# Kernel tuning notes

Hardware: AMD Instinct MI355X
Metric: run time of the kernel (lower is better)

Reference implementation:

```python
import jax, jax.numpy as jnp
import numpy as np

B, K, H, W = 8, 4, 256, 256
HID = 16
DT, STEPS, JITERS, OMEGA = 0.1, 12, 8, 0.9
D_MAX, CHI_MAX, K_MAX = 2.0, 2.0, 1.0


def _conv2d(x, w, b):
    y = jax.lax.conv_general_dilated(x, w, (1, 1), 'SAME',
                                     dimension_numbers=('NCHW', 'OIHW', 'NCHW'))
    return y + b[None, :, None, None]


def _pad(x):  # replicate pad by 1 on H, W
    return jnp.pad(x, ((0, 0), (0, 0), (1, 1), (1, 1)), mode='edge')


def laplacian(x):
    xp = _pad(x)
    return (xp[:, :, :-2, 1:-1] + xp[:, :, 2:, 1:-1]
            + xp[:, :, 1:-1, :-2] + xp[:, :, 1:-1, 2:] - 4.0 * x)


def gradient(x):
    xp = _pad(x)
    gx = xp[:, :, 1:-1, 2:] - x   # forward diff along W
    gy = xp[:, :, 2:, 1:-1] - x   # forward diff along H
    return gx, gy


def divergence(vx, vy):
    xp = _pad(vx)
    yp = _pad(vy)
    dvx = vx - xp[:, :, 1:-1, 2:]
    dvy = vy - yp[:, :, 2:, 1:-1]
    return dvx + dvy


def project_simplex(p, eps=1e-8):
    # p: [..., K]; faithful port incl. the rho-1 indexing of the torch code
    Kc = p.shape[-1]
    x = jnp.nan_to_num(p)
    u = jnp.flip(jnp.sort(x, axis=-1), axis=-1)            # descending
    cssv = jnp.cumsum(u, axis=-1) - 1.0
    ind = jnp.arange(1, Kc + 1, dtype=x.dtype)
    cond = (u - cssv / ind) > 0
    rho = jnp.argmax(cond.astype(jnp.int32) * jnp.arange(1, Kc + 1), axis=-1)
    rho_idx = jnp.maximum(rho - 1, 0)[..., None]
    tau = jnp.take_along_axis(cssv, rho_idx, axis=-1) / jnp.maximum(rho_idx + 1, 1)
    tau = jnp.nan_to_num(tau)
    w = jnp.maximum(x - tau, 0.0)
    return w / (w.sum(-1, keepdims=True) + eps)


def setup_inputs() -> dict:
    key = jax.random.key(0)
    ks = jax.random.split(key, 8)
    p0 = jax.random.uniform(ks[0], (B, K, H, W), dtype=jnp.float32)
    p0 = p0 / p0.sum(1, keepdims=True)
    w1 = jax.random.normal(ks[1], (HID, K, 3, 3), jnp.float32) * np.sqrt(2.0 / (K * 9))
    w2 = jax.random.normal(ks[2], (HID, HID, 3, 3), jnp.float32) * np.sqrt(2.0 / (HID * 9))
    w3 = jax.random.normal(ks[3], (1, HID, 1, 1), jnp.float32) * np.sqrt(1.0 / HID)
    return {
        'p0': p0,
        'D_raw': jnp.full((K,), 0.5, jnp.float32),
        'chi_raw': jnp.float32(0.5),
        'k_tumor_raw': jnp.float32(0.3),
        'cap_tumor_logit': jnp.float32(np.log(0.7) - np.log(0.3)),
        'w1': w1, 'b1': jnp.zeros((HID,), jnp.float32),
        'w2': w2, 'b2': jnp.zeros((HID,), jnp.float32),
        'w3': w3, 'b3': jnp.zeros((1,), jnp.float32),
        'tumor_idx': 0,
    }


def _forward(p0, D_raw, chi_raw, k_tumor_raw, cap_tumor_logit,
             w1, b1, w2, b2, w3, b3, tumor_idx):
    ti = int(tumor_idx)
    sp = jax.nn.softplus
    D_all = jnp.minimum(sp(D_raw) + 1e-8, D_MAX)                 # [K]
    chi = jnp.minimum(sp(chi_raw) + 1e-8, CHI_MAX)
    k_t = jnp.minimum(sp(k_tumor_raw) + 1e-8, K_MAX)             # unused in tumor_map mode
    cap_t = jnp.clip(jax.nn.sigmoid(cap_tumor_logit), 0.001, 0.95)

    # GrowthCNN (k_mode='tumor_map')
    h = jax.nn.relu(_conv2d(p0, w1, b1))
    h = jax.nn.relu(_conv2d(h, w2, b2))
    k_map = jnp.maximum(jax.nn.sigmoid(_conv2d(h, w3, b3)) * K_MAX, 1e-6)  # [B,1,H,W]

    D4 = D_all[None, :, None, None]
    diag = 1.0 + DT * D4 * 4.0

    p = jnp.maximum(jnp.nan_to_num(p0), 0.0)
    for _ in range(STEPS):
        gx, gy = gradient(p)
        gx = jnp.nan_to_num(gx)
        gy = jnp.nan_to_num(gy)
        sum_gx = gx.sum(1, keepdims=True)
        sum_gy = gy.sum(1, keepdims=True)
        fx = jnp.nan_to_num(-chi * p * (sum_gx - gx))
        fy = jnp.nan_to_num(-chi * p * (sum_gy - gy))
        cross = jnp.nan_to_num(divergence(fx, fy))

        pt = jnp.clip(p[:, ti:ti + 1], 0.0, 1.0)
        rt = jnp.nan_to_num(k_map * pt * (1.0 - pt / cap_t))
        react = jnp.zeros_like(p).at[:, ti:ti + 1].set(rt)

        rhs = jnp.nan_to_num(p + DT * (cross + react))

        # damped Jacobi for implicit diffusion, vectorized over channels
        xk = p
        for _it in range(JITERS):
            Lx = laplacian(xk)
            r = rhs - (xk - DT * D4 * Lx)
            xk = jnp.nan_to_num(xk + (OMEGA / diag) * r)

        p = project_simplex(jnp.moveaxis(xk, 1, -1))
        p = jnp.maximum(jnp.nan_to_num(jnp.moveaxis(p, -1, 1)), 0.0)
    return p


def reference(p0, D_raw, chi_raw, k_tumor_raw, cap_tumor_logit,
              w1, b1, w2, b2, w3, b3, tumor_idx):
    return _forward(p0, D_raw, chi_raw, k_tumor_raw, cap_tumor_logit,
                    w1, b1, w2, b2, w3, b3, tumor_idx)


if __name__ == '__main__':
    out = reference(**setup_inputs())
    print(out.shape, out.dtype)
```

## Files before the change

### kernel.cpp

```cpp
#include <hip/hip_runtime.h>
#include <math.h>

#define B_ 8
#define K4 4
#define H_ 256
#define W_ 256
#define HID_ 16
#define DT_ 0.1f
#define STEPS_ 12
#define OMEGA_ 0.9f
#define D_MAX_ 2.0f
#define CHI_MAX_ 2.0f
#define HW_ (H_ * W_)

__device__ __forceinline__ int clampi(int v, int lo, int hi) { return min(max(v, lo), hi); }

__device__ __forceinline__ float softplus_f(float x) {
    return fmaxf(x, 0.0f) + log1pf(expf(-fabsf(x)));
}

__device__ __forceinline__ void proj4(float v0, float v1, float v2, float v3,
                                      float& o0, float& o1, float& o2, float& o3) {
    float u0 = v0, u1 = v1, u2 = v2, u3 = v3, t;
    t = fmaxf(u0, u1); u1 = fminf(u0, u1); u0 = t;
    t = fmaxf(u2, u3); u3 = fminf(u2, u3); u2 = t;
    t = fmaxf(u0, u2); u2 = fminf(u0, u2); u0 = t;
    t = fmaxf(u1, u3); u3 = fminf(u1, u3); u1 = t;
    t = fmaxf(u1, u2); u2 = fminf(u1, u2); u1 = t;
    float cs1 = u0 + u1;
    float cs2 = cs1 + u2;
    float c0 = u0 - 1.0f;
    float c1 = cs1 - 1.0f;
    float c2 = cs2 - 1.0f;
    int rho = 0;
    if (u1 - c1 / 2.0f > 0.0f) rho = 1;
    if (u2 - c2 / 3.0f > 0.0f) rho = 2;
    if (u3 - (cs2 + u3 - 1.0f) / 4.0f > 0.0f) rho = 3;
    int ri = rho - 1; if (ri < 0) ri = 0;
    float tau = (ri == 0) ? c0 : (ri == 1) ? (c1 / 2.0f) : (c2 / 3.0f);
    float w0 = fmaxf(v0 - tau, 0.0f);
    float w1 = fmaxf(v1 - tau, 0.0f);
    float w2 = fmaxf(v2 - tau, 0.0f);
    float w3 = fmaxf(v3 - tau, 0.0f);
    float inv = 1.0f / (w0 + w1 + w2 + w3 + 1e-8f);
    o0 = w0 * inv; o1 = w1 * inv; o2 = w2 * inv; o3 = w3 * inv;
}

__global__ void setup_kernel(const float* __restrict__ D_raw,
                             const float* __restrict__ chi_raw,
                             const float* __restrict__ cap_logit,
                             const float* __restrict__ w1,
                             const float* __restrict__ w2,
                             float* __restrict__ params,
                             float* __restrict__ w1t,
                             float* __restrict__ w2t) {
    int tid = threadIdx.x;
    if (tid == 0) {
        for (int c = 0; c < K4; ++c) {
            float d = fminf(softplus_f(D_raw[c]) + 1e-8f, D_MAX_);
            params[c]      = d;
            params[6 + c]  = DT_ * d;
            params[10 + c] = OMEGA_ / (1.0f + DT_ * d * 4.0f);
        }
        params[4] = fminf(softplus_f(chi_raw[0]) + 1e-8f, CHI_MAX_);
        float ct = 1.0f / (1.0f + expf(-cap_logit[0]));
        params[5] = fminf(fmaxf(ct, 0.001f), 0.95f);
    }
    for (int i = tid; i < 576; i += 256) {
        int o = i & 15, rest = i >> 4, ic = rest / 9, k = rest % 9;
        w1t[i] = w1[(o * K4 + ic) * 9 + k];
    }
    for (int i = tid; i < 2304; i += 256) {
        int o = i & 15, rest = i >> 4, ic = rest / 9, k = rest % 9;
        w2t[i] = w2[(o * HID_ + ic) * 9 + k];
    }
}

#define PS2_(c,ry,rx) csmem[((c)*20 + (ry))*24 + (rx)]
#define HS2_(o,ry,rx) csmem[1920 + ((o)*18 + (ry))*21 + (rx)]
#define PSUM_ (1920 + 6048)

__global__ __launch_bounds__(512) void cnn_kernel(const float* __restrict__ p0,
                                                  const float* __restrict__ w1t,
                                                  const float* __restrict__ b1,
                                                  const float* __restrict__ w2t,
                                                  const float* __restrict__ b2,
                                                  const float* __restrict__ w3,
                                                  const float* __restrict__ b3,
                                                  float* __restrict__ kmap) {
    __shared__ float csmem[1920 + 6048 + 512];
    const int tid = threadIdx.x;
    const int tx0 = blockIdx.x * 16, ty0 = blockIdx.y * 16, b = blockIdx.z;

    for (int i = tid; i < 4 * 20 * 20; i += 512) {
        int c = i / 400, r = i % 400;
        int ry = r / 20, rx = r % 20;
        int gy = ty0 + ry - 2, gx = tx0 + rx - 2;
        float v = 0.0f;
        if ((unsigned)gy < 256u && (unsigned)gx < 256u)
            v = p0[(((size_t)b * K4 + c) << 16) + gy * W_ + gx];
        PS2_(c, ry, rx) = v;
    }
    __syncthreads();

    if (tid < 18 * 18) {
        int iy = tid / 18, ixx = tid % 18;
        int gy = ty0 + iy - 1, gx = tx0 + ixx - 1;
        bool indom = ((unsigned)gy < 256u) && ((unsigned)gx < 256u);
        float acc[HID_];
#pragma unroll
        for (int o = 0; o < HID_; ++o) acc[o] = b1[o];
        for (int ic = 0; ic < K4; ++ic)
            for (int ky = 0; ky < 3; ++ky)
#pragma unroll
                for (int kx = 0; kx < 3; ++kx) {
                    float v = PS2_(ic, iy + ky, ixx + kx);
                    const float* wp = w1t + (ic * 9 + ky * 3 + kx) * 16;
#pragma unroll
                    for (int o = 0; o < HID_; ++o)
                        acc[o] = fmaf(wp[o], v, acc[o]);
                }
#pragma unroll
        for (int o = 0; o < HID_; ++o)
            HS2_(o, iy, ixx) = indom ? fmaxf(acc[o], 0.0f) : 0.0f;
    }
    __syncthreads();

    {
        int px = tid & 255;
        int hb = __builtin_amdgcn_readfirstlane((tid >> 8) & 1) * 8;
        int iy2 = px >> 4, ix2 = px & 15;
        float acc[8];
#pragma unroll
        for (int o = 0; o < 8; ++o) acc[o] = b2[hb + o];
        for (int ic = 0; ic < HID_; ++ic)
            for (int ky = 0; ky < 3; ++ky)
#pragma unroll
                for (int kx = 0; kx < 3; ++kx) {
                    float v = HS2_(ic, iy2 + ky, ix2 + kx);
                    const float* wp = w2t + (ic * 9 + ky * 3 + kx) * 16 + hb;
#pragma unroll
                    for (int o = 0; o < 8; ++o)
                        acc[o] = fmaf(wp[o], v, acc[o]);
                }
        float s = 0.0f;
#pragma unroll
        for (int o = 0; o < 8; ++o)
            s += w3[hb + o] * fmaxf(acc[o], 0.0f);
        csmem[PSUM_ + (tid >> 8) * 256 + px] = s;
    }
    __syncthreads();

    if (tid < 256) {
        int iy2 = tid >> 4, ix2 = tid & 15;
        float s = b3[0] + csmem[PSUM_ + tid] + csmem[PSUM_ + 256 + tid];
        float km = 1.0f / (1.0f + expf(-s));
        km = fmaxf(km, 1e-6f);
        kmap[((size_t)b << 16) + (ty0 + iy2) * W_ + tx0 + ix2] = km;
    }
}

#define PP_(c,ry,rx) psm[((c)*18 + (ry))*20 + (rx)]

__global__ __launch_bounds__(256) void proj_rhs_kernel(const float* __restrict__ xin,
                                                       const float* __restrict__ kmap,
                                                       const float* __restrict__ params,
                                                       const int* __restrict__ tumor_idx,
                                                       float* __restrict__ pout,
                                                       float* __restrict__ rhs,
                                                       int mode) {
    const int tid = threadIdx.x;
    const int tx0 = blockIdx.x * 16, ty0 = blockIdx.y * 16, b = blockIdx.z;

    if (mode == 2) {
        int ry = tid >> 4, rx = tid & 15;
        size_t off = ((size_t)(b * K4) << 16) + (ty0 + ry) * W_ + tx0 + rx;
        float v0 = xin[off];
        float v1 = xin[off + HW_];
        float v2 = xin[off + 2 * HW_];
        float v3 = xin[off + 3 * HW_];
        proj4(v0, v1, v2, v3, v0, v1, v2, v3);
        pout[off]           = v0;
        pout[off + HW_]     = v1;
        pout[off + 2 * HW_] = v2;
        pout[off + 3 * HW_] = v3;
        return;
    }

    __shared__ float psm[4 * 18 * 20];

    for (int i = tid; i < 18 * 18; i += 256) {
        int ry = i / 18, rx = i % 18;
        int gy = clampi(ty0 + ry, 0, 255);
        int gx = clampi(tx0 + rx, 0, 255);
        size_t off = (((size_t)b * K4) << 16) + gy * W_ + gx;
        float v0 = xin[off], v1 = xin[off + HW_];
        float v2 = xin[off + 2 * HW_], v3 = xin[off + 3 * HW_];
        if (mode == 0) {
            v0 = fmaxf(v0, 0.0f); v1 = fmaxf(v1, 0.0f);
            v2 = fmaxf(v2, 0.0f); v3 = fmaxf(v3, 0.0f);
        } else {
            proj4(v0, v1, v2, v3, v0, v1, v2, v3);
        }
        PP_(0, ry, rx) = v0; PP_(1, ry, rx) = v1;
        PP_(2, ry, rx) = v2; PP_(3, ry, rx) = v3;
    }
    __syncthreads();

    const float chi = params[4], cap = params[5];
    const int ti = tumor_idx[0];
    int ry = tid >> 4, rx = tid & 15;
    int gy = ty0 + ry, gx = tx0 + rx;
    int row1 = clampi(gy + 1, 0, 255) - ty0;
    int row2 = clampi(gy + 2, 0, 255) - ty0;
    int col1 = clampi(gx + 1, 0, 255) - tx0;
    int col2 = clampi(gx + 2, 0, 255) - tx0;
    float pc[4], px1[4], py1[4], g0x[4], g1x[4], g0y[4], g1y[4];
    float s0x = 0.f, s1x = 0.f, s0y = 0.f, s1y = 0.f;
#pragma unroll
    for (int c = 0; c < 4; ++c) {
        float pcv = PP_(c, ry, rx);
        float a   = PP_(c, ry, col1);
        float bb  = PP_(c, ry, col2);
        float d   = PP_(c, row1, rx);
        float e   = PP_(c, row2, rx);
        pc[c] = pcv; px1[c] = a; py1[c] = d;
        g0x[c] = a - pcv;  g1x[c] = bb - a;
        g0y[c] = d - pcv;  g1y[c] = e - d;
        s0x += g0x[c]; s1x += g1x[c]; s0y += g0y[c]; s1y += g1y[c];
    }
    float km = kmap[((size_t)b << 16) + gy * W_ + gx];
    size_t off = (((size_t)b * K4) << 16) + gy * W_ + gx;
#pragma unroll
    for (int c = 0; c < 4; ++c) {
        float fx0 = -chi * pc[c]  * (s0x - g0x[c]);
        float fx1 = -chi * px1[c] * (s1x - g1x[c]);
        float fy0 = -chi * pc[c]  * (s0y - g0y[c]);
        float fy1 = -chi * py1[c] * (s1y - g1y[c]);
        float cross = (fx0 - fx1) + (fy0 - fy1);
        float react = 0.0f;
        if (c == ti) {
            float pt = fminf(fmaxf(pc[c], 0.0f), 1.0f);
            react = km * pt * (1.0f - pt / cap);
        }
        rhs[off + (size_t)c * HW_]  = pc[c] + DT_ * (cross + react);
        pout[off + (size_t)c * HW_] = pc[c];
    }
}

#define JXSTR 88
#define JX_(buf,row,col) jsm[(buf)*(50*JXSTR) + (row)*JXSTR + (col)]

__global__ __launch_bounds__(1024, 8) void jacobi8_kernel(const float* __restrict__ p,
                                                          const float* __restrict__ rhs,
                                                          const float* __restrict__ params,
                                                          float* __restrict__ xk) {
    __shared__ float jsm[2 * 50 * JXSTR];
    const int tid = threadIdx.x;
    const int tx0 = blockIdx.x * 64, ty0 = blockIdx.y * 32;
    const int bc = blockIdx.z;
    const int c  = bc & 3;
    const float* pc_ = p + ((size_t)bc << 16);

    for (int i = tid; i < 48 * 80; i += 1024) {
        int r = i / 80, x = i % 80;
        int gy = clampi(ty0 + r - 8, 0, 255);
        int gx = clampi(tx0 + x - 8, 0, 255);
        JX_(0, r + 1, x + 4) = pc_[gy * W_ + gx];
    }

    const bool act = (tid < 960);
    const int ry_it = tid / 20, g = tid % 20;
    const int gy = ty0 + ry_it - 8;
    const int gx0 = tx0 + 4 * g - 8;
    const int yc = ry_it + 1;
    const int yu = clampi(gy - 1, 0, 255) - ty0 + 9;
    const int yd = clampi(gy + 1, 0, 255) - ty0 + 9;
    const int ix = 4 + 4 * g;
    const bool lm = (gx0 == 0), rm = (gx0 == 252);
    const float dtD = params[6 + c];
    const float wod = params[10 + c];

    float4 rsv;
    if (act) {
        const float* rr = rhs + ((size_t)bc << 16) + clampi(gy, 0, 255) * W_;
        if (gx0 >= 0 && gx0 <= 252) {
            rsv = *(const float4*)&rr[gx0];
        } else {
            rsv.x = rr[clampi(gx0,     0, 255)];
            rsv.y = rr[clampi(gx0 + 1, 0, 255)];
            rsv.z = rr[clampi(gx0 + 2, 0, 255)];
            rsv.w = rr[clampi(gx0 + 3, 0, 255)];
        }
    }
    __syncthreads();

    float4 ce;
    if (act) ce = *(const float4*)&JX_(0, yc, ix);

#pragma unroll
    for (int j = 0; j < 8; ++j) {
        const int rb = j & 1;
        float4 ov;
        if (act) {
            float4 up = *(const float4*)&JX_(rb, yu, ix);
            float4 dn = *(const float4*)&JX_(rb, yd, ix);
            float lf = JX_(rb, yc, ix - 1);
            float rt = JX_(rb, yc, ix + 4);
            float l0 = lm ? ce.x : lf;
            float r3 = rm ? ce.w : rt;
            {
                float lap = up.x + dn.x + l0 + ce.y - 4.0f * ce.x;
                float r = rsv.x - (ce.x - dtD * lap);
                ov.x = ce.x + wod * r;
            }
            {
                float lap = up.y + dn.y + ce.x + ce.z - 4.0f * ce.y;
                float r = rsv.y - (ce.y - dtD * lap);
                ov.y = ce.y + wod * r;
            }
            {
                float lap = up.z + dn.z + ce.y + ce.w - 4.0f * ce.z;
                float r = rsv.z - (ce.z - dtD * lap);
                ov.z = ce.z + wod * r;
            }
            {
                float lap = up.w + dn.w + ce.z + r3 - 4.0f * ce.w;
                float r = rsv.w - (ce.w - dtD * lap);
                ov.w = ce.w + wod * r;
            }
        }
        if (j < 7) {
            if (act) *(float4*)&JX_((rb ^ 1), yc, ix) = ov;
            __syncthreads();
        }
        if (act) ce = ov;
    }

    if (act && ry_it >= 8 && ry_it < 40 && g >= 2 && g < 18)
        *(float4*)&xk[((size_t)bc << 16) + gy * W_ + gx0] = ce;
}

extern "C" void kernel_launch(void* const* d_in, const int* in_sizes, int n_in,
                              void* d_out, int out_size, void* d_ws, size_t ws_size,
                              hipStream_t stream) {
    const float* p0        = (const float*)d_in[0];
    const float* D_raw     = (const float*)d_in[1];
    const float* chi_raw   = (const float*)d_in[2];
    const float* cap_logit = (const float*)d_in[4];
    const float* w1        = (const float*)d_in[5];
    const float* b1        = (const float*)d_in[6];
    const float* w2        = (const float*)d_in[7];
    const float* b2        = (const float*)d_in[8];
    const float* w3        = (const float*)d_in[9];
    const float* b3        = (const float*)d_in[10];
    const int*   tumor_idx = (const int*)d_in[11];

    char* ws = (char*)d_ws;
    float* params = (float*)(ws + 0);
    float* w1t    = (float*)(ws + 1024);
    float* w2t    = (float*)(ws + 4096);
    float* kmap   = (float*)(ws + 65536);
    float* p      = (float*)(ws + 4  * 1024 * 1024);
    float* rhs    = (float*)(ws + 12 * 1024 * 1024);
    float* xk     = (float*)d_out;

    setup_kernel<<<1, 256, 0, stream>>>(D_raw, chi_raw, cap_logit, w1, w2,
                                        params, w1t, w2t);
    dim3 cgrid(16, 16, B_);
    cnn_kernel<<<cgrid, 512, 0, stream>>>(p0, w1t, b1, w2t, b2, w3, b3, kmap);

    dim3 pgrid(16, 16, B_);
    dim3 jgrid(4, 8, B_ * K4);
    for (int s = 0; s < STEPS_; ++s) {
        const float* xin = (s == 0) ? p0 : xk;
        proj_rhs_kernel<<<pgrid, 256, 0, stream>>>(xin, kmap, params, tumor_idx,
                                                   p, rhs, s == 0 ? 0 : 1);
        jacobi8_kernel<<<jgrid, 1024, 0, stream>>>(p, rhs, params, xk);
    }
    proj_rhs_kernel<<<pgrid, 256, 0, stream>>>(xk, kmap, params, tumor_idx,
                                               xk, rhs, 2);
}
```

Baseline: 392.9 us.

## Enlarge Jacobi tile to 64x64 with two work items per thread

Doubles the Jacobi block's tile height so each block processes an 80x80 halo region, with each thread handling up to two float4 cells. This lowers the fraction of redundant halo recomputation from the 8-sweep temporal blocking and halves the number of blocks. In exchange, shared memory per block roughly doubles and the grid shrinks, which may reduce occupancy and parallelism.

After: 360.6 us. -8.2%, faster.

```diff
diff --git a/kernel.cpp b/kernel.cpp
--- a/kernel.cpp
+++ b/kernel.cpp
@@ -248,97 +248,135 @@
     }
 }
 
-#define JXSTR 88
-#define JX_(buf,row,col) jsm[(buf)*(50*JXSTR) + (row)*JXSTR + (col)]
+#define JROWS 82
+#define JSTR 88
+#define JX_(buf,row,col) jsm[(buf)*(JROWS*JSTR) + (row)*JSTR + (col)]
+
+__device__ __forceinline__ float4 jac_sweep64(const float* rp, float4 ce, float4 rsv,
+                                              int yc, int yu, int yd, int ix,
+                                              bool lm, bool rm, float dtD, float wod) {
+    float4 up = *(const float4*)&rp[yu * JSTR + ix];
+    float4 dn = *(const float4*)&rp[yd * JSTR + ix];
+    float lf = rp[yc * JSTR + ix - 1];
+    float rt = rp[yc * JSTR + ix + 4];
+    float l0 = lm ? ce.x : lf;
+    float r3 = rm ? ce.w : rt;
+    float4 ov;
+    {
+        float lap = up.x + dn.x + l0 + ce.y - 4.0f * ce.x;
+        float r = rsv.x - (ce.x - dtD * lap);
+        ov.x = ce.x + wod * r;
+    }
+    {
+        float lap = up.y + dn.y + ce.x + ce.z - 4.0f * ce.y;
+        float r = rsv.y - (ce.y - dtD * lap);
+        ov.y = ce.y + wod * r;
+    }
+    {
+        float lap = up.z + dn.z + ce.y + ce.w - 4.0f * ce.z;
+        float r = rsv.z - (ce.z - dtD * lap);
+        ov.z = ce.z + wod * r;
+    }
+    {
+        float lap = up.w + dn.w + ce.z + r3 - 4.0f * ce.w;
+        float r = rsv.w - (ce.w - dtD * lap);
+        ov.w = ce.w + wod * r;
+    }
+    return ov;
+}
 
 __global__ __launch_bounds__(1024, 8) void jacobi8_kernel(const float* __restrict__ p,
                                                           const float* __restrict__ rhs,
                                                           const float* __restrict__ params,
                                                           float* __restrict__ xk) {
-    __shared__ float jsm[2 * 50 * JXSTR];
+    __shared__ float jsm[2 * JROWS * JSTR];
     const int tid = threadIdx.x;
-    const int tx0 = blockIdx.x * 64, ty0 = blockIdx.y * 32;
+    const int tx0 = blockIdx.x * 64, ty0 = blockIdx.y * 64;
     const int bc = blockIdx.z;
     const int c  = bc & 3;
     const float* pc_ = p + ((size_t)bc << 16);
 
-    for (int i = tid; i < 48 * 80; i += 1024) {
+    for (int i = tid; i < 80 * 80; i += 1024) {
         int r = i / 80, x = i % 80;
         int gy = clampi(ty0 + r - 8, 0, 255);
         int gx = clampi(tx0 + x - 8, 0, 255);
         JX_(0, r + 1, x + 4) = pc_[gy * W_ + gx];
     }
 
-    const bool act = (tid < 960);
-    const int ry_it = tid / 20, g = tid % 20;
-    const int gy = ty0 + ry_it - 8;
-    const int gx0 = tx0 + 4 * g - 8;
-    const int yc = ry_it + 1;
-    const int yu = clampi(gy - 1, 0, 255) - ty0 + 9;
-    const int yd = clampi(gy + 1, 0, 255) - ty0 + 9;
-    const int ix = 4 + 4 * g;
-    const bool lm = (gx0 == 0), rm = (gx0 == 252);
     const float dtD = params[6 + c];
     const float wod = params[10 + c];
-
-    float4 rsv;
-    if (act) {
-        const float* rr = rhs + ((size_t)bc << 16) + clampi(gy, 0, 255) * W_;
-        if (gx0 >= 0 && gx0 <= 252) {
-            rsv = *(const float4*)&rr[gx0];
+    const float* rbase = rhs + ((size_t)bc << 16);
+
+    const int ryA = tid / 20, gA = tid % 20;
+    const int gyA = ty0 + ryA - 8;
+    const int gx0A = tx0 + 4 * gA - 8;
+    const int ycA = ryA + 1;
+    const int yuA = clampi(gyA - 1, 0, 255) - ty0 + 9;
+    const int ydA = clampi(gyA + 1, 0, 255) - ty0 + 9;
+    const int ixA = 4 + 4 * gA;
+    const bool lmA = (gx0A == 0), rmA = (gx0A == 252);
+
+    const bool hasB = (tid < 576);
+    const int itB = tid + 1024;
+    const int ryB = itB / 20, gB = itB % 20;
+    const int gyB = ty0 + ryB - 8;
+    const int gx0B = tx0 + 4 * gB - 8;
+    const int ycB = ryB + 1;
+    const int yuB = clampi(gyB - 1, 0, 255) - ty0 + 9;
+    const int ydB = clampi(gyB + 1, 0, 255) - ty0 + 9;
+    const int ixB = 4 + 4 * gB;
+    const bool lmB = (gx0B == 0), rmB = (gx0B == 252);
+
+    float4 rsvA, rsvB;
+    {
+        const float* rr = rbase + clampi(gyA, 0, 255) * W_;
+        if (gx0A >= 0 && gx0A <= 252) {
+            rsvA = *(const float4*)&rr[gx0A];
         } else {
-            rsv.x = rr[clampi(gx0,     0, 255)];
-            rsv.y = rr[clampi(gx0 + 1, 0, 255)];
-            rsv.z = rr[clampi(gx0 + 2, 0, 255)];
-            rsv.w = rr[clampi(gx0 + 3, 0, 255)];
+            rsvA.x = rr[clampi(gx0A,     0, 255)];
+            rsvA.y = rr[clampi(gx0A + 1, 0, 255)];
+            rsvA.z = rr[clampi(gx0A + 2, 0, 255)];
+            rsvA.w = rr[clampi(gx0A + 3, 0, 255)];
+        }
+    }
+    if (hasB) {
+        const float* rr = rbase + clampi(gyB, 0, 255) * W_;
+        if (gx0B >= 0 && gx0B <= 252) {
+            rsvB = *(const float4*)&rr[gx0B];
+        } else {
+            rsvB.x = rr[clampi(gx0B,     0, 255)];
+            rsvB.y = rr[clampi(gx0B + 1, 0, 255)];
+            rsvB.z = rr[clampi(gx0B + 2, 0, 255)];
+            rsvB.w = rr[clampi(gx0B + 3, 0, 255)];
         }
     }
     __syncthreads();
 
-    float4 ce;
-    if (act) ce = *(const float4*)&JX_(0, yc, ix);
+    float4 ceA = *(const float4*)&JX_(0, ycA, ixA);
+    float4 ceB;
+    if (hasB) ceB = *(const float4*)&JX_(0, ycB, ixB);
 
 #pragma unroll
     for (int j = 0; j < 8; ++j) {
         const int rb = j & 1;
-        float4 ov;
-        if (act) {
-            float4 up = *(const float4*)&JX_(rb, yu, ix);
-            float4 dn = *(const float4*)&JX_(rb, yd, ix);
-            float lf = JX_(rb, yc, ix - 1);
-            float rt = JX_(rb, yc, ix + 4);
-            float l0 = lm ? ce.x : lf;
-            float r3 = rm ? ce.w : rt;
-            {
-                float lap = up.x + dn.x + l0 + ce.y - 4.0f * ce.x;
-                float r = rsv.x - (ce.x - dtD * lap);
-                ov.x = ce.x + wod * r;
-            }
-            {
-                float lap = up.y + dn.y + ce.x + ce.z - 4.0f * ce.y;
-                float r = rsv.y - (ce.y - dtD * lap);
-                ov.y = ce.y + wod * r;
-            }
-            {
-                float lap = up.z + dn.z + ce.y + ce.w - 4.0f * ce.z;
-                float r = rsv.z - (ce.z - dtD * lap);
-                ov.z = ce.z + wod * r;
-            }
-            {
-                float lap = up.w + dn.w + ce.z + r3 - 4.0f * ce.w;
-                float r = rsv.w - (ce.w - dtD * lap);
-                ov.w = ce.w + wod * r;
-            }
-        }
+        const float* rp = &jsm[rb * (JROWS * JSTR)];
+        float* wpb = &jsm[(rb ^ 1) * (JROWS * JSTR)];
+        float4 ovA = jac_sweep64(rp, ceA, rsvA, ycA, yuA, ydA, ixA, lmA, rmA, dtD, wod);
+        float4 ovB;
+        if (hasB) ovB = jac_sweep64(rp, ceB, rsvB, ycB, yuB, ydB, ixB, lmB, rmB, dtD, wod);
         if (j < 7) {
-            if (act) *(float4*)&JX_((rb ^ 1), yc, ix) = ov;
+            *(float4*)&wpb[ycA * JSTR + ixA] = ovA;
+            if (hasB) *(float4*)&wpb[ycB * JSTR + ixB] = ovB;
             __syncthreads();
         }
-        if (act) ce = ov;
-    }
-
-    if (act && ry_it >= 8 && ry_it < 40 && g >= 2 && g < 18)
-        *(float4*)&xk[((size_t)bc << 16) + gy * W_ + gx0] = ce;
+        ceA = ovA;
+        if (hasB) ceB = ovB;
+    }
+
+    if (ryA >= 8 && ryA < 72 && gA >= 2 && gA < 18)
+        *(float4*)&xk[((size_t)bc << 16) + gyA * W_ + gx0A] = ceA;
+    if (hasB && ryB >= 8 && ryB < 72 && gB >= 2 && gB < 18)
+        *(float4*)&xk[((size_t)bc << 16) + gyB * W_ + gx0B] = ceB;
 }
 
 extern "C" void kernel_launch(void* const* d_in, const int* in_sizes, int n_in,
@@ -371,7 +409,7 @@
     cnn_kernel<<<cgrid, 512, 0, stream>>>(p0, w1t, b1, w2t, b2, w3, b3, kmap);
 
     dim3 pgrid(16, 16, B_);
-    dim3 jgrid(4, 8, B_ * K4);
+    dim3 jgrid(4, 4, B_ * K4);
     for (int s = 0; s < STEPS_; ++s) {
         const float* xin = (s == 0) ? p0 : xk;
         proj_rhs_kernel<<<pgrid, 256, 0, stream>>>(xin, kmap, params, tumor_idx,
```
